# Optimization experiments

Hardware: AMD Instinct MI355X
Metric: run time of the kernel (lower is better)

The kernel has to match this reference:

```python
import jax, jax.numpy as jnp
import numpy as np

N, E, B, IN, H = 20000, 50000, 1024, 32, 64

def setup_inputs() -> dict:
    key = jax.random.key(0)
    ks = jax.random.split(key, 32)
    d = {}
    d["x"] = jax.random.normal(ks[0], (N, IN), jnp.float32)
    d["edge_index"] = jax.random.randint(ks[1], (2, E), 0, N)
    d["edge_attr"] = jax.random.uniform(ks[2], (E, 6), dtype=jnp.float32)
    d["batch"] = jnp.sort(jax.random.randint(ks[3], (N,), 0, B))
    d["t"] = jax.random.uniform(ks[4], (B, 1), dtype=jnp.float32)
    d["p"] = jax.random.uniform(ks[5], (B, 1), dtype=jnp.float32)
    d["num_graphs"] = B
    def lin(k, fan_in, shape):
        return jax.random.normal(k, shape, jnp.float32) * (1.0 / np.sqrt(fan_in))
    # lin0: IN -> H
    d["W0"] = lin(ks[6], IN, (IN, H)); d["b0"] = jnp.zeros((H,), jnp.float32)
    # edge MLP: 6 -> 64 -> H*H
    d["We1"] = lin(ks[7], 6, (6, 64)); d["be1"] = jnp.zeros((64,), jnp.float32)
    d["We2"] = lin(ks[8], 64, (64, H * H)); d["be2"] = jnp.zeros((H * H,), jnp.float32)
    # NNConv root weight + bias
    d["Wroot"] = lin(ks[9], H, (H, H)); d["bconv"] = jnp.zeros((H,), jnp.float32)
    # GRU (input H, hidden H), torch layout [3H, *] gate order r,z,n
    d["gru_wih"] = lin(ks[10], H, (3 * H, H)); d["gru_whh"] = lin(ks[11], H, (3 * H, H))
    d["gru_bih"] = jnp.zeros((3 * H,), jnp.float32); d["gru_bhh"] = jnp.zeros((3 * H,), jnp.float32)
    # Set2Set LSTM (input 2H, hidden H), torch layout [4H, *] gate order i,f,g,o
    d["l_wih"] = lin(ks[12], 2 * H, (4 * H, 2 * H)); d["l_whh"] = lin(ks[13], H, (4 * H, H))
    d["l_bih"] = jnp.zeros((4 * H,), jnp.float32); d["l_bhh"] = jnp.zeros((4 * H,), jnp.float32)
    # readout MLP
    d["W1"] = lin(ks[14], 2 * H + 2, (2 * H + 2, H)); d["b1"] = jnp.zeros((H,), jnp.float32)
    d["W2"] = lin(ks[15], H, (H, 64)); d["b2"] = jnp.zeros((64,), jnp.float32)
    d["W3"] = lin(ks[16], 64, (64, 1)); d["b3"] = jnp.zeros((1,), jnp.float32)
    return d


def reference(x, edge_attr, t, p, W0, b0, We1, be1, We2, be2, Wroot, bconv,
              gru_wih, gru_whh, gru_bih, gru_bhh, l_wih, l_whh, l_bih, l_bhh,
              W1, b1, W2, b2, W3, b3, edge_index, batch, num_graphs):
    n_nodes = x.shape[0]
    hdim = W0.shape[1]
    src, dst = edge_index[0], edge_index[1]

    out = jax.nn.relu(x @ W0 + b0)            # [N,H]
    h = out

    # edge MLP -> per-edge weight matrices [E,H,H] (edge_attr is loop-invariant)
    ew = (jax.nn.relu(edge_attr @ We1 + be1) @ We2 + be2).reshape(-1, hdim, hdim)

    for _ in range(4):
        # NNConv: gather source features, per-edge matmul, scatter-add to targets
        msg = jnp.einsum('eh,eho->eo', out[src], ew)                 # [E,H]
        agg = jax.ops.segment_sum(msg, dst, num_segments=n_nodes)    # [N,H]
        m = jax.nn.relu(agg + out @ Wroot + bconv)
        # GRU step (single timestep)
        gi = m @ gru_wih.T + gru_bih
        gh = h @ gru_whh.T + gru_bhh
        ir, iz, inn = jnp.split(gi, 3, axis=-1)
        hr, hz, hn = jnp.split(gh, 3, axis=-1)
        r = jax.nn.sigmoid(ir + hr)
        z = jax.nn.sigmoid(iz + hz)
        nn_ = jnp.tanh(inn + r * hn)
        h = (1.0 - z) * nn_ + z * h
        out = h

    # Set2Set pooling, 3 processing steps
    qh = jnp.zeros((num_graphs, hdim), x.dtype)
    qc = jnp.zeros((num_graphs, hdim), x.dtype)
    q_star = jnp.zeros((num_graphs, 2 * hdim), x.dtype)
    for _ in range(3):
        g = q_star @ l_wih.T + l_bih + qh @ l_whh.T + l_bhh
        gi_, gf_, gg_, go_ = jnp.split(g, 4, axis=-1)
        qc = jax.nn.sigmoid(gf_) * qc + jax.nn.sigmoid(gi_) * jnp.tanh(gg_)
        qh = jax.nn.sigmoid(go_) * jnp.tanh(qc)
        q = qh                                                        # [B,H]
        e = jnp.sum(out * q[batch], axis=-1, keepdims=True)          # [N,1]
        emax = jax.ops.segment_max(e, batch, num_segments=num_graphs)
        a = jnp.exp(e - emax[batch])
        asum = jax.ops.segment_sum(a, batch, num_segments=num_graphs)
        a = a / asum[batch]                                           # segment softmax
        r_ = jax.ops.segment_sum(a * out, batch, num_segments=num_graphs)
        q_star = jnp.concatenate([q, r_], axis=-1)

    feat = jnp.concatenate([q_star, t, p], axis=-1)                   # [B,2H+2]
    y = jax.nn.relu(feat @ W1 + b1)
    y = jax.nn.relu(y @ W2 + b2)
    y = y @ W3 + b3
    return y.reshape(-1)
```

## Files before the change

kernel.cpp:

```cpp
#include <hip/hip_runtime.h>
#include <math.h>

#define N_NODES 20000
#define N_EDGES 50000
#define NB      1024
#define IND     32
#define HDIM    64

typedef __attribute__((ext_vector_type(8))) short bf16x8;
typedef __attribute__((ext_vector_type(4))) float f32x4;

static inline size_t align_up(size_t x, size_t a) { return (x + a - 1) & ~(a - 1); }

__device__ __forceinline__ float sigmoidf_(float x) {
    return 1.0f / (1.0f + __expf(-x));
}
__device__ __forceinline__ float tanhf_(float x) {
    float xc = fminf(fmaxf(x, -15.0f), 15.0f);
    float e = __expf(2.0f * xc);
    return (e - 1.0f) / (e + 1.0f);
}
__device__ __forceinline__ unsigned pk2(float p0, float p1) {
    unsigned u0 = __float_as_uint(p0) + 0x8000u;
    unsigned u1 = __float_as_uint(p1) + 0x8000u;
    return __builtin_amdgcn_perm(u1, u0, 0x07060302u);
}
__device__ __forceinline__ unsigned bf1(float v) {
    return (__float_as_uint(v) + 0x8000u) >> 16;
}

__global__ void k_prep(const float* __restrict__ We2, const float* __restrict__ be2,
                       short* __restrict__ We2b,
                       const float* __restrict__ Wroot, const float* __restrict__ gwhh,
                       const float* __restrict__ gwih,
                       short* __restrict__ WB1h, short* __restrict__ WB1l,
                       short* __restrict__ WB2h, short* __restrict__ WB2l,
                       const float* __restrict__ lwih, const float* __restrict__ lwhh,
                       float* __restrict__ lwihT, float* __restrict__ lwhhT,
                       const int* __restrict__ batch, int* __restrict__ offs) {
    int bid = blockIdx.x, tid = threadIdx.x;
    if (bid < 1040) {
        int idx = bid * 256 + tid;
        int s = idx >> 12;
        int col = idx & 4095;
        int k = col >> 6, o = col & 63;
        float val = (s < 64) ? We2[k * 4096 + s * 64 + o] : be2[k * 64 + o];
        int dst = s * 4096 + (((o >> 4) * 128 + (k >> 5) * 64 + ((k >> 3) & 3) * 16 + (o & 15)) << 3) + (k & 7);
        We2b[dst] = (short)bf1(val);
    } else if (bid < 1152) {
        int idx = (bid - 1040) * 256 + tid;
        if (idx < 28672) {
            bool b1 = idx < 16384;
            int li = b1 ? idx : idx - 16384;
            int j = li & 7, lane = (li >> 3) & 63, c = (li >> 9) & 1, otile = li >> 10;
            int k = c * 32 + (lane >> 4) * 8 + j;
            int o = otile * 16 + (lane & 15);
            float val;
            if (b1) val = (o < 64) ? Wroot[k * 64 + o] : gwhh[(o - 64) * 64 + k];
            else    val = gwih[o * 64 + k];
            unsigned hs = bf1(val);
            float lo = val - __uint_as_float(hs << 16);
            unsigned ls = bf1(lo);
            if (b1) { WB1h[li] = (short)hs; WB1l[li] = (short)ls; }
            else    { WB2h[li] = (short)hs; WB2l[li] = (short)ls; }
        }
    } else if (bid < 1280) {
        int idx = (bid - 1152) * 256 + tid;
        int i = idx >> 8, j = idx & 255;
        lwihT[idx] = lwih[j * 128 + i];
    } else if (bid < 1344) {
        int idx = (bid - 1280) * 256 + tid;
        int i = idx >> 8, j = idx & 255;
        lwhhT[idx] = lwhh[j * 64 + i];
    } else {
        int i = (bid - 1344) * 256 + tid;
        if (i <= NB) {
            int lo = 0, hi = N_NODES;
            while (lo < hi) { int mid = (lo + hi) >> 1; if (batch[mid] < i) lo = mid + 1; else hi = mid; }
            offs[i] = lo;
        }
    }
}

__global__ void k_count(const int* __restrict__ ei, int* __restrict__ deg) {
    int e = blockIdx.x * 256 + threadIdx.x;
    if (e < N_EDGES) atomicAdd(&deg[ei[N_EDGES + e]], 1);
}

__global__ void k_scan(const int* __restrict__ deg, int* __restrict__ rowptr, int* __restrict__ cursor) {
    __shared__ int s_w[16];
    int t = threadIdx.x;
    int base = t * 20;
    int v[20]; int s = 0;
#pragma unroll
    for (int i = 0; i < 20; ++i) {
        int idx = base + i;
        v[i] = (idx < N_NODES) ? deg[idx] : 0;
        s += v[i];
    }
    int lane = t & 63, w = t >> 6;
    int inc = s;
#pragma unroll
    for (int off = 1; off < 64; off <<= 1) {
        int o = __shfl_up(inc, off);
        if (lane >= off) inc += o;
    }
    if (lane == 63) s_w[w] = inc;
    __syncthreads();
    if (w == 0 && lane < 16) {
        int x = s_w[lane];
        int xs = x;
#pragma unroll
        for (int off = 1; off < 16; off <<= 1) {
            int o = __shfl_up(xs, off);
            if (lane >= off) xs += o;
        }
        s_w[lane] = xs - x;
    }
    __syncthreads();
    int run = s_w[w] + (inc - s);
#pragma unroll
    for (int i = 0; i < 20; ++i) {
        int idx = base + i;
        if (idx < N_NODES) { rowptr[idx] = run; cursor[idx] = run; }
        else if (idx == N_NODES) rowptr[idx] = run;
        run += v[i];
    }
}

__global__ void k_fill(const int* __restrict__ ei, int* __restrict__ cursor, int* __restrict__ perm) {
    int e = blockIdx.x * 256 + threadIdx.x;
    if (e < N_EDGES) {
        int pos = atomicAdd(&cursor[ei[N_EDGES + e]], 1);
        perm[pos] = e;
    }
}

__global__ void k_init_feat(const float* __restrict__ x, const float* __restrict__ W0,
                            const float* __restrict__ b0, float* __restrict__ hbuf,
                            const float* __restrict__ ea, const float* __restrict__ We1,
                            const float* __restrict__ be1, float* __restrict__ re) {
    int bid = blockIdx.x;
    int tid = threadIdx.x;
    int w = tid >> 6, j = tid & 63;
    if (bid < 5000) {
        int n = bid * 4 + w;
        float acc = b0[j];
        const float* xr = x + n * IND;
#pragma unroll
        for (int i = 0; i < IND; ++i) acc = fmaf(xr[i], W0[i * 64 + j], acc);
        hbuf[n * 64 + j] = fmaxf(acc, 0.0f);
    } else {
        int e = (bid - 5000) * 4 + w;
        if (e >= N_EDGES) return;
        float acc = be1[j];
        const float* er = ea + e * 6;
#pragma unroll
        for (int i = 0; i < 6; ++i) acc = fmaf(er[i], We1[i * 64 + j], acc);
        re[e * 64 + j] = fmaxf(acc, 0.0f);
    }
}

__launch_bounds__(256, 3)
__global__ void k_msg_mfma(const float* __restrict__ hbuf, const float* __restrict__ reb,
                           const short* __restrict__ We2b, const int* __restrict__ ei,
                           float* __restrict__ msg) {
    __shared__ float s_v[64][64];
    int tid = threadIdx.x;
    int eb = blockIdx.x * 64;
    int lane = tid & 63;
    int w = tid >> 6;
    int l15 = lane & 15, lhi = lane >> 4;

    {
        int se = tid >> 2;
        int sh = tid & 3;
        int ge = eb + se;
        const float* rowp = (ge < N_EDGES) ? (hbuf + (size_t)ei[ge] * 64) : (const float*)0;
#pragma unroll
        for (int rr4 = 0; rr4 < 4; ++rr4) {
            int hb = rr4 * 16 + sh * 4;
            float4 vv = rowp ? *(const float4*)(rowp + hb) : make_float4(0.f, 0.f, 0.f, 0.f);
            s_v[hb + 0][se] = vv.x; s_v[hb + 1][se] = vv.y;
            s_v[hb + 2][se] = vv.z; s_v[hb + 3][se] = vv.w;
        }
    }

    union U { int4 i4; bf16x8 v; };
    U a_re[4][2];
#pragma unroll
    for (int m = 0; m < 4; ++m) {
        int ge = eb + m * 16 + l15;
        if (ge < N_EDGES) {
            const float* rp = reb + (size_t)ge * 64 + lhi * 8;
            float4 x0 = *(const float4*)(rp);
            float4 x1 = *(const float4*)(rp + 4);
            float4 y0 = *(const float4*)(rp + 32);
            float4 y1 = *(const float4*)(rp + 36);
            a_re[m][0].i4 = make_int4(pk2(x0.x, x0.y), pk2(x0.z, x0.w), pk2(x1.x, x1.y), pk2(x1.z, x1.w));
            a_re[m][1].i4 = make_int4(pk2(y0.x, y0.y), pk2(y0.z, y0.w), pk2(y1.x, y1.y), pk2(y1.z, y1.w));
        } else {
            a_re[m][0].i4 = make_int4(0, 0, 0, 0);
            a_re[m][1].i4 = make_int4(0, 0, 0, 0);
        }
    }

    const int4* bp0 = (const int4*)We2b + (w * 128 + lane);
    const int4* bp1 = bp0 + 64;
    int4 Sc0[4], Sc1[4];
#pragma unroll
    for (int j = 0; j < 4; ++j) {
        Sc0[j] = bp0[j * 512];
        Sc1[j] = bp1[j * 512];
    }

    __syncthreads();

    const f32x4 zero4 = {0.f, 0.f, 0.f, 0.f};
    f32x4 macc[4];
#pragma unroll
    for (int m = 0; m < 4; ++m) macc[m] = zero4;

    float4 vv[4], vn[4];
#pragma unroll
    for (int m = 0; m < 4; ++m) vv[m] = *(const float4*)&s_v[0][m * 16 + lhi * 4];

    for (int g = 0; g < 16; ++g) {
#pragma unroll
        for (int j = 0; j < 4; ++j) {
            int s = g * 4 + j;
            int snext = (s < 63) ? (s + 1) : 63;
#pragma unroll
            for (int m = 0; m < 4; ++m)
                vn[m] = *(const float4*)&s_v[snext][m * 16 + lhi * 4];
            U bb0, bb1; bb0.i4 = Sc0[j]; bb1.i4 = Sc1[j];
#pragma unroll
            for (int m = 0; m < 4; ++m) {
                f32x4 t = __builtin_amdgcn_mfma_f32_16x16x32_bf16(a_re[m][0].v, bb0.v, zero4, 0, 0, 0);
                t = __builtin_amdgcn_mfma_f32_16x16x32_bf16(a_re[m][1].v, bb1.v, t, 0, 0, 0);
                macc[m][0] = fmaf(vv[m].x, t[0], macc[m][0]);
                macc[m][1] = fmaf(vv[m].y, t[1], macc[m][1]);
                macc[m][2] = fmaf(vv[m].z, t[2], macc[m][2]);
                macc[m][3] = fmaf(vv[m].w, t[3], macc[m][3]);
            }
            int sload = (s + 4 <= 64) ? (s + 4) : 64;
            Sc0[j] = bp0[sload * 512];
            Sc1[j] = bp1[sload * 512];
#pragma unroll
            for (int m = 0; m < 4; ++m) vv[m] = vn[m];
        }
    }

    {
        U bb0, bb1; bb0.i4 = Sc0[0]; bb1.i4 = Sc1[0];
#pragma unroll
        for (int m = 0; m < 4; ++m) {
            int e = m * 16 + l15;
            U a0, a1;
            a0.i4 = make_int4(
                pk2(s_v[lhi * 8 + 0][e], s_v[lhi * 8 + 1][e]),
                pk2(s_v[lhi * 8 + 2][e], s_v[lhi * 8 + 3][e]),
                pk2(s_v[lhi * 8 + 4][e], s_v[lhi * 8 + 5][e]),
                pk2(s_v[lhi * 8 + 6][e], s_v[lhi * 8 + 7][e]));
            a1.i4 = make_int4(
                pk2(s_v[32 + lhi * 8 + 0][e], s_v[32 + lhi * 8 + 1][e]),
                pk2(s_v[32 + lhi * 8 + 2][e], s_v[32 + lhi * 8 + 3][e]),
                pk2(s_v[32 + lhi * 8 + 4][e], s_v[32 + lhi * 8 + 5][e]),
                pk2(s_v[32 + lhi * 8 + 6][e], s_v[32 + lhi * 8 + 7][e]));
            macc[m] = __builtin_amdgcn_mfma_f32_16x16x32_bf16(a0.v, bb0.v, macc[m], 0, 0, 0);
            macc[m] = __builtin_amdgcn_mfma_f32_16x16x32_bf16(a1.v, bb1.v, macc[m], 0, 0, 0);
        }
    }
    int o = w * 16 + l15;
#pragma unroll
    for (int m = 0; m < 4; ++m) {
#pragma unroll
        for (int r = 0; r < 4; ++r) {
            int el = m * 16 + lhi * 4 + r;
            int ge = eb + el;
            if (ge < N_EDGES) msg[(size_t)ge * 64 + o] = macc[m][r];
        }
    }
}

__launch_bounds__(256, 4)
__global__ void k_node_update(float* __restrict__ hbuf, const float* __restrict__ msg,
                              const int* __restrict__ rowptr, const int* __restrict__ perm,
                              const short* __restrict__ WB1h, const short* __restrict__ WB1l,
                              const short* __restrict__ WB2h, const short* __restrict__ WB2l,
                              const float* __restrict__ bconv, const float* __restrict__ bih,
                              const float* __restrict__ bhh) {
    __shared__ short s_hh[32][72];
    __shared__ short s_hl[32][72];
    __shared__ short s_mh[32][72];
    __shared__ short s_ml[32][72];
    __shared__ float s_agg[32][68];
    int tid = threadIdx.x;
    int nbase = blockIdx.x * 32;
    int lane = tid & 63, w = tid >> 6;
    int l15 = lane & 15, lhi = lane >> 4;

    {
        int nt = tid >> 3, q = tid & 7;
        int n = nbase + nt;
#pragma unroll
        for (int c4 = 0; c4 < 2; ++c4) {
            int col = q * 8 + c4 * 4;
            float4 v = *(const float4*)&hbuf[(size_t)n * 64 + col];
            unsigned h01 = pk2(v.x, v.y), h23 = pk2(v.z, v.w);
            float f0 = __uint_as_float(h01 << 16);
            float f1 = __uint_as_float(h01 & 0xffff0000u);
            float f2 = __uint_as_float(h23 << 16);
            float f3 = __uint_as_float(h23 & 0xffff0000u);
            unsigned l01 = pk2(v.x - f0, v.y - f1), l23 = pk2(v.z - f2, v.w - f3);
            *(unsigned*)&s_hh[nt][col]     = h01;
            *(unsigned*)&s_hh[nt][col + 2] = h23;
            *(unsigned*)&s_hl[nt][col]     = l01;
            *(unsigned*)&s_hl[nt][col + 2] = l23;
        }
        float4 aggv[2];
#pragma unroll
        for (int c4 = 0; c4 < 2; ++c4)
            aggv[c4] = *(const float4*)&bconv[q * 8 + c4 * 4];
        int rs = rowptr[n], rend = rowptr[n + 1];
        for (int qq = rs; qq < rend; ++qq) {
            const float* mrow = msg + (size_t)perm[qq] * 64 + q * 8;
#pragma unroll
            for (int c4 = 0; c4 < 2; ++c4) {
                float4 mv = *(const float4*)&mrow[c4 * 4];
                aggv[c4].x += mv.x; aggv[c4].y += mv.y;
                aggv[c4].z += mv.z; aggv[c4].w += mv.w;
            }
        }
#pragma unroll
        for (int c4 = 0; c4 < 2; ++c4)
            *(float4*)&s_agg[nt][q * 8 + c4 * 4] = aggv[c4];
    }
    __syncthreads();

    union U { int4 i4; bf16x8 v; };
    U ah[2][2], al[2][2];
#pragma unroll
    for (int m = 0; m < 2; ++m)
#pragma unroll
        for (int c = 0; c < 2; ++c) {
            ah[m][c].i4 = *(const int4*)&s_hh[m * 16 + l15][c * 32 + lhi * 8];
            al[m][c].i4 = *(const int4*)&s_hl[m * 16 + l15][c * 32 + lhi * 8];
        }

    const int4* B1h = (const int4*)WB1h;
    const int4* B1l = (const int4*)WB1l;
    const int4* B2h = (const int4*)WB2h;
    const int4* B2l = (const int4*)WB2l;

    f32x4 C0[2], G[3][2], I[3][2];

    {
        int ot = w;
        U bh0, bh1, bl0, bl1;
        bh0.i4 = B1h[(ot * 2 + 0) * 64 + lane];
        bh1.i4 = B1h[(ot * 2 + 1) * 64 + lane];
        bl0.i4 = B1l[(ot * 2 + 0) * 64 + lane];
        bl1.i4 = B1l[(ot * 2 + 1) * 64 + lane];
#pragma unroll
        for (int m = 0; m < 2; ++m) {
            f32x4 c;
#pragma unroll
            for (int r = 0; r < 4; ++r) c[r] = s_agg[m * 16 + lhi * 4 + r][w * 16 + l15];
            c = __builtin_amdgcn_mfma_f32_16x16x32_bf16(ah[m][0].v, bh0.v, c, 0, 0, 0);
            c = __builtin_amdgcn_mfma_f32_16x16x32_bf16(ah[m][1].v, bh1.v, c, 0, 0, 0);
            c = __builtin_amdgcn_mfma_f32_16x16x32_bf16(al[m][0].v, bh0.v, c, 0, 0, 0);
            c = __builtin_amdgcn_mfma_f32_16x16x32_bf16(al[m][1].v, bh1.v, c, 0, 0, 0);
            c = __builtin_amdgcn_mfma_f32_16x16x32_bf16(ah[m][0].v, bl0.v, c, 0, 0, 0);
            c = __builtin_amdgcn_mfma_f32_16x16x32_bf16(ah[m][1].v, bl1.v, c, 0, 0, 0);
            C0[m] = c;
        }
    }
#pragma unroll
    for (int m = 0; m < 2; ++m)
#pragma unroll
        for (int r = 0; r < 4; ++r) {
            float mv = fmaxf(C0[m][r], 0.0f);
            int row = m * 16 + lhi * 4 + r, col = w * 16 + l15;
            unsigned hs = bf1(mv);
            float lof = mv - __uint_as_float(hs << 16);
            s_mh[row][col] = (short)hs;
            s_ml[row][col] = (short)bf1(lof);
        }
#pragma unroll
    for (int p = 1; p < 4; ++p) {
        int ot = p * 4 + w;
        U bh0, bh1, bl0, bl1;
        bh0.i4 = B1h[(ot * 2 + 0) * 64 + lane];
        bh1.i4 = B1h[(ot * 2 + 1) * 64 + lane];
        bl0.i4 = B1l[(ot * 2 + 0) * 64 + lane];
        bl1.i4 = B1l[(ot * 2 + 1) * 64 + lane];
        float bv = bhh[(p - 1) * 64 + w * 16 + l15];
#pragma unroll
        for (int m = 0; m < 2; ++m) {
            f32x4 c = {bv, bv, bv, bv};
            c = __builtin_amdgcn_mfma_f32_16x16x32_bf16(ah[m][0].v, bh0.v, c, 0, 0, 0);
            c = __builtin_amdgcn_mfma_f32_16x16x32_bf16(ah[m][1].v, bh1.v, c, 0, 0, 0);
            c = __builtin_amdgcn_mfma_f32_16x16x32_bf16(al[m][0].v, bh0.v, c, 0, 0, 0);
            c = __builtin_amdgcn_mfma_f32_16x16x32_bf16(al[m][1].v, bh1.v, c, 0, 0, 0);
            c = __builtin_amdgcn_mfma_f32_16x16x32_bf16(ah[m][0].v, bl0.v, c, 0, 0, 0);
            c = __builtin_amdgcn_mfma_f32_16x16x32_bf16(ah[m][1].v, bl1.v, c, 0, 0, 0);
            G[p - 1][m] = c;
        }
    }
    __syncthreads();
    U mh[2][2], ml[2][2];
#pragma unroll
    for (int m = 0; m < 2; ++m)
#pragma unroll
        for (int c = 0; c < 2; ++c) {
            mh[m][c].i4 = *(const int4*)&s_mh[m * 16 + l15][c * 32 + lhi * 8];
            ml[m][c].i4 = *(const int4*)&s_ml[m * 16 + l15][c * 32 + lhi * 8];
        }
#pragma unroll
    for (int p = 0; p < 3; ++p) {
        int ot = p * 4 + w;
        U bh0, bh1, bl0, bl1;
        bh0.i4 = B2h[(ot * 2 + 0) * 64 + lane];
        bh1.i4 = B2h[(ot * 2 + 1) * 64 + lane];
        bl0.i4 = B2l[(ot * 2 + 0) * 64 + lane];
        bl1.i4 = B2l[(ot * 2 + 1) * 64 + lane];
        float bv = bih[p * 64 + w * 16 + l15];
#pragma unroll
        for (int m = 0; m < 2; ++m) {
            f32x4 c = {bv, bv, bv, bv};
            c = __builtin_amdgcn_mfma_f32_16x16x32_bf16(mh[m][0].v, bh0.v, c, 0, 0, 0);
            c = __builtin_amdgcn_mfma_f32_16x16x32_bf16(mh[m][1].v, bh1.v, c, 0, 0, 0);
            c = __builtin_amdgcn_mfma_f32_16x16x32_bf16(ml[m][0].v, bh0.v, c, 0, 0, 0);
            c = __builtin_amdgcn_mfma_f32_16x16x32_bf16(ml[m][1].v, bh1.v, c, 0, 0, 0);
            c = __builtin_amdgcn_mfma_f32_16x16x32_bf16(mh[m][0].v, bl0.v, c, 0, 0, 0);
            c = __builtin_amdgcn_mfma_f32_16x16x32_bf16(mh[m][1].v, bl1.v, c, 0, 0, 0);
            I[p][m] = c;
        }
    }
#pragma unroll
    for (int m = 0; m < 2; ++m)
#pragma unroll
        for (int r = 0; r < 4; ++r) {
            int row = m * 16 + lhi * 4 + r;
            int n = nbase + row;
            int col = w * 16 + l15;
            float hold = __uint_as_float(((unsigned)(unsigned short)s_hh[row][col]) << 16)
                       + __uint_as_float(((unsigned)(unsigned short)s_hl[row][col]) << 16);
            float rg = sigmoidf_(I[0][m][r] + G[0][m][r]);
            float z  = sigmoidf_(I[1][m][r] + G[1][m][r]);
            float nn = tanhf_(I[2][m][r] + rg * G[2][m][r]);
            hbuf[(size_t)n * 64 + col] = (1.0f - z) * nn + z * hold;
        }
}

__launch_bounds__(256)
__global__ void k_set2set(const float* __restrict__ hbuf, const int* __restrict__ offs,
                          const float* __restrict__ t, const float* __restrict__ p,
                          const float* __restrict__ lwihT, const float* __restrict__ lwhhT,
                          const float* __restrict__ l_bih, const float* __restrict__ l_bhh,
                          const float* __restrict__ W1, const float* __restrict__ b1,
                          const float* __restrict__ W2, const float* __restrict__ b2,
                          const float* __restrict__ W3, const float* __restrict__ b3,
                          float* __restrict__ y) {
    __shared__ float s_qs[192];
    __shared__ float s_g[256];
    __shared__ float s_racc[4][64];
    __shared__ float s_m[4], s_l[4];
    __shared__ float s_y[64];
    int b = blockIdx.x;
    int tid = threadIdx.x;
    int w = tid >> 6, lane = tid & 63;
    int s = offs[b], e = offs[b + 1];
    float bi = l_bih[tid] + l_bhh[tid];
    float qc = 0.f;

    if (tid < 192) s_qs[tid] = 0.f;
    __syncthreads();

    for (int iter = 0; iter < 3; ++iter) {
        float g = bi;
#pragma unroll 8
        for (int i = 0; i < 128; ++i) g = fmaf(s_qs[i], lwihT[i * 256 + tid], g);
#pragma unroll 8
        for (int i = 0; i < 64; ++i)  g = fmaf(s_qs[128 + i], lwhhT[i * 256 + tid], g);
        s_g[tid] = g;
        __syncthreads();
        if (w == 0) {
            float ci = sigmoidf_(s_g[lane]);
            float cf = sigmoidf_(s_g[64 + lane]);
            float cg = tanhf_(s_g[128 + lane]);
            float co = sigmoidf_(s_g[192 + lane]);
            qc = cf * qc + ci * cg;
            float qh = co * tanhf_(qc);
            s_qs[lane] = qh;
            s_qs[128 + lane] = qh;
        }
        __syncthreads();
        float qv = s_qs[128 + lane];
        float mx = -1e30f, l = 0.0f, racc = 0.0f;
        for (int n = s + w; n < e; n += 4) {
            float xv = hbuf[(size_t)n * 64 + lane];
            float prod = xv * qv;
#pragma unroll
            for (int off = 32; off > 0; off >>= 1) prod += __shfl_xor(prod, off);
            float mnew = fmaxf(mx, prod);
            float scale = __expf(mx - mnew);
            float wgt = __expf(prod - mnew);
            l = l * scale + wgt;
            racc = racc * scale + wgt * xv;
            mx = mnew;
        }
        s_racc[w][lane] = racc;
        if (lane == 0) { s_m[w] = mx; s_l[w] = l; }
        __syncthreads();
        if (w == 0) {
            float M = fmaxf(fmaxf(s_m[0], s_m[1]), fmaxf(s_m[2], s_m[3]));
            float L = 0.f, R = 0.f;
#pragma unroll
            for (int ww = 0; ww < 4; ++ww) {
                float sc = __expf(s_m[ww] - M);
                L += s_l[ww] * sc;
                R = fmaf(s_racc[ww][lane], sc, R);
            }
            s_qs[64 + lane] = (e > s) ? (R / L) : 0.0f;
        }
        __syncthreads();
    }
    if (w == 0) {
        float acc = b1[lane];
#pragma unroll 8
        for (int i = 0; i < 128; ++i) acc = fmaf(s_qs[i], W1[i * 64 + lane], acc);
        acc = fmaf(t[b], W1[128 * 64 + lane], acc);
        acc = fmaf(p[b], W1[129 * 64 + lane], acc);
        acc = fmaxf(acc, 0.0f);
        s_y[lane] = acc;
        float acc2 = b2[lane];
#pragma unroll 8
        for (int i = 0; i < 64; ++i) acc2 = fmaf(s_y[i], W2[i * 64 + lane], acc2);
        acc2 = fmaxf(acc2, 0.0f);
        float part = acc2 * W3[lane];
#pragma unroll
        for (int off = 32; off > 0; off >>= 1) part += __shfl_xor(part, off);
        if (lane == 0) y[b] = part + b3[0];
    }
}

extern "C" void kernel_launch(void* const* d_in, const int* in_sizes, int n_in,
                              void* d_out, int out_size, void* d_ws, size_t ws_size,
                              hipStream_t stream) {
    const float* x     = (const float*)d_in[0];
    const int*   ei    = (const int*)  d_in[1];
    const float* ea    = (const float*)d_in[2];
    const int*   batch = (const int*)  d_in[3];
    const float* t     = (const float*)d_in[4];
    const float* p     = (const float*)d_in[5];
    const float* W0    = (const float*)d_in[7];
    const float* b0    = (const float*)d_in[8];
    const float* We1   = (const float*)d_in[9];
    const float* be1   = (const float*)d_in[10];
    const float* We2   = (const float*)d_in[11];
    const float* be2   = (const float*)d_in[12];
    const float* Wroot = (const float*)d_in[13];
    const float* bconv = (const float*)d_in[14];
    const float* gwih  = (const float*)d_in[15];
    const float* gwhh  = (const float*)d_in[16];
    const float* gbih  = (const float*)d_in[17];
    const float* gbhh  = (const float*)d_in[18];
    const float* lwih  = (const float*)d_in[19];
    const float* lwhh  = (const float*)d_in[20];
    const float* lbih  = (const float*)d_in[21];
    const float* lbhh  = (const float*)d_in[22];
    const float* W1    = (const float*)d_in[23];
    const float* b1    = (const float*)d_in[24];
    const float* W2    = (const float*)d_in[25];
    const float* b2    = (const float*)d_in[26];
    const float* W3    = (const float*)d_in[27];
    const float* b3    = (const float*)d_in[28];
    float* y = (float*)d_out;

    char* ws = (char*)d_ws;
    size_t off = 0;
    auto alloc = [&](size_t nbytes) {
        void* ptr = (void*)(ws + off);
        off += align_up(nbytes, 256);
        return ptr;
    };
    float* hbuf   = (float*)alloc((size_t)N_NODES * 64 * 4);
    float* reb    = (float*)alloc((size_t)N_EDGES * 64 * 4);
    float* msg    = (float*)alloc((size_t)N_EDGES * 64 * 4);
    short* We2b   = (short*)alloc((size_t)65 * 4096 * 2);
    short* WB1h   = (short*)alloc(16384 * 2);
    short* WB1l   = (short*)alloc(16384 * 2);
    short* WB2h   = (short*)alloc(12288 * 2);
    short* WB2l   = (short*)alloc(12288 * 2);
    float* lwihT  = (float*)alloc(32768 * 4);
    float* lwhhT  = (float*)alloc(16384 * 4);
    int*   offs   = (int*)  alloc((NB + 1) * 4);
    int*   deg    = (int*)  alloc(N_NODES * 4);
    int*   rowptr = (int*)  alloc((N_NODES + 1) * 4);
    int*   cursor = (int*)  alloc(N_NODES * 4);
    int*   perm   = (int*)  alloc(N_EDGES * 4);

    k_prep<<<1349, 256, 0, stream>>>(We2, be2, We2b, Wroot, gwhh, gwih,
                                     WB1h, WB1l, WB2h, WB2l,
                                     lwih, lwhh, lwihT, lwhhT, batch, offs);
    hipMemsetAsync(deg, 0, (size_t)N_NODES * 4, stream);
    k_count<<<(N_EDGES + 255) / 256, 256, 0, stream>>>(ei, deg);
    k_scan<<<1, 1024, 0, stream>>>(deg, rowptr, cursor);
    k_fill<<<(N_EDGES + 255) / 256, 256, 0, stream>>>(ei, cursor, perm);

    k_init_feat<<<17500, 256, 0, stream>>>(x, W0, b0, hbuf, ea, We1, be1, reb);

    for (int it = 0; it < 4; ++it) {
        k_msg_mfma<<<(N_EDGES + 63) / 64, 256, 0, stream>>>(hbuf, reb, We2b, ei, msg);
        k_node_update<<<N_NODES / 32, 256, 0, stream>>>(hbuf, msg, rowptr, perm,
                                                        WB1h, WB1l, WB2h, WB2l,
                                                        bconv, gbih, gbhh);
    }

    k_set2set<<<NB, 256, 0, stream>>>(hbuf, offs, t, p, lwihT, lwhhT, lbih, lbhh,
                                      W1, b1, W2, b2, W3, b3, y);
}
```

Baseline: 414.1 us.

## Split message kernel reduction over hidden dim across two blocks with partial buffers

The per-edge message kernel now launches two blocks per 64-edge tile. Each block handles half of the 64 input hidden slices, and only one half adds the bias slab. The two partial messages are written to separate buffers, and the node update kernel sums both during aggregation. This doubles the parallelism of the MFMA-heavy message kernel, at the cost of duplicated gather and edge-feature loads per tile, an extra message buffer write, and double the message reads in node update.

```diff
diff --git a/kernel.cpp b/kernel.cpp
--- a/kernel.cpp
+++ b/kernel.cpp
@@ -164,10 +164,12 @@
 __launch_bounds__(256, 3)
 __global__ void k_msg_mfma(const float* __restrict__ hbuf, const float* __restrict__ reb,
                            const short* __restrict__ We2b, const int* __restrict__ ei,
-                           float* __restrict__ msg) {
+                           float* __restrict__ msgA, float* __restrict__ msgB) {
     __shared__ float s_v[64][64];
     int tid = threadIdx.x;
-    int eb = blockIdx.x * 64;
+    int tile = blockIdx.x >> 1;
+    int half = blockIdx.x & 1;
+    int eb = tile * 64;
     int lane = tid & 63;
     int w = tid >> 6;
     int l15 = lane & 15, lhi = lane >> 4;
@@ -205,13 +207,14 @@
         }
     }
 
+    int hbase = half * 32;
     const int4* bp0 = (const int4*)We2b + (w * 128 + lane);
     const int4* bp1 = bp0 + 64;
     int4 Sc0[4], Sc1[4];
 #pragma unroll
     for (int j = 0; j < 4; ++j) {
-        Sc0[j] = bp0[j * 512];
-        Sc1[j] = bp1[j * 512];
+        Sc0[j] = bp0[(size_t)(hbase + j) * 512];
+        Sc1[j] = bp1[(size_t)(hbase + j) * 512];
     }
 
     __syncthreads();
@@ -223,13 +226,13 @@
 
     float4 vv[4], vn[4];
 #pragma unroll
-    for (int m = 0; m < 4; ++m) vv[m] = *(const float4*)&s_v[0][m * 16 + lhi * 4];
-
-    for (int g = 0; g < 16; ++g) {
+    for (int m = 0; m < 4; ++m) vv[m] = *(const float4*)&s_v[hbase][m * 16 + lhi * 4];
+
+    for (int g = 0; g < 8; ++g) {
 #pragma unroll
         for (int j = 0; j < 4; ++j) {
             int s = g * 4 + j;
-            int snext = (s < 63) ? (s + 1) : 63;
+            int snext = (s < 31) ? (hbase + s + 1) : (hbase + 31);
 #pragma unroll
             for (int m = 0; m < 4; ++m)
                 vn[m] = *(const float4*)&s_v[snext][m * 16 + lhi * 4];
@@ -243,15 +246,16 @@
                 macc[m][2] = fmaf(vv[m].z, t[2], macc[m][2]);
                 macc[m][3] = fmaf(vv[m].w, t[3], macc[m][3]);
             }
-            int sload = (s + 4 <= 64) ? (s + 4) : 64;
-            Sc0[j] = bp0[sload * 512];
-            Sc1[j] = bp1[sload * 512];
+            int gslab = hbase + s + 4;
+            if (gslab > 64) gslab = 64;
+            Sc0[j] = bp0[(size_t)gslab * 512];
+            Sc1[j] = bp1[(size_t)gslab * 512];
 #pragma unroll
             for (int m = 0; m < 4; ++m) vv[m] = vn[m];
         }
     }
 
-    {
+    if (half == 1) {
         U bb0, bb1; bb0.i4 = Sc0[0]; bb1.i4 = Sc1[0];
 #pragma unroll
         for (int m = 0; m < 4; ++m) {
@@ -271,6 +275,7 @@
             macc[m] = __builtin_amdgcn_mfma_f32_16x16x32_bf16(a1.v, bb1.v, macc[m], 0, 0, 0);
         }
     }
+    float* mout = half ? msgB : msgA;
     int o = w * 16 + l15;
 #pragma unroll
     for (int m = 0; m < 4; ++m) {
@@ -278,13 +283,14 @@
         for (int r = 0; r < 4; ++r) {
             int el = m * 16 + lhi * 4 + r;
             int ge = eb + el;
-            if (ge < N_EDGES) msg[(size_t)ge * 64 + o] = macc[m][r];
+            if (ge < N_EDGES) mout[(size_t)ge * 64 + o] = macc[m][r];
         }
     }
 }
 
 __launch_bounds__(256, 4)
-__global__ void k_node_update(float* __restrict__ hbuf, const float* __restrict__ msg,
+__global__ void k_node_update(float* __restrict__ hbuf, const float* __restrict__ msgA,
+                              const float* __restrict__ msgB,
                               const int* __restrict__ rowptr, const int* __restrict__ perm,
                               const short* __restrict__ WB1h, const short* __restrict__ WB1l,
                               const short* __restrict__ WB2h, const short* __restrict__ WB2l,
@@ -324,12 +330,15 @@
             aggv[c4] = *(const float4*)&bconv[q * 8 + c4 * 4];
         int rs = rowptr[n], rend = rowptr[n + 1];
         for (int qq = rs; qq < rend; ++qq) {
-            const float* mrow = msg + (size_t)perm[qq] * 64 + q * 8;
+            size_t mbase = (size_t)perm[qq] * 64 + q * 8;
+            const float* mrowA = msgA + mbase;
+            const float* mrowB = msgB + mbase;
 #pragma unroll
             for (int c4 = 0; c4 < 2; ++c4) {
-                float4 mv = *(const float4*)&mrow[c4 * 4];
-                aggv[c4].x += mv.x; aggv[c4].y += mv.y;
-                aggv[c4].z += mv.z; aggv[c4].w += mv.w;
+                float4 ma = *(const float4*)&mrowA[c4 * 4];
+                float4 mb = *(const float4*)&mrowB[c4 * 4];
+                aggv[c4].x += ma.x + mb.x; aggv[c4].y += ma.y + mb.y;
+                aggv[c4].z += ma.z + mb.z; aggv[c4].w += ma.w + mb.w;
             }
         }
 #pragma unroll
@@ -588,7 +597,8 @@
     };
     float* hbuf   = (float*)alloc((size_t)N_NODES * 64 * 4);
     float* reb    = (float*)alloc((size_t)N_EDGES * 64 * 4);
-    float* msg    = (float*)alloc((size_t)N_EDGES * 64 * 4);
+    float* msgA   = (float*)alloc((size_t)N_EDGES * 64 * 4);
+    float* msgB   = (float*)alloc((size_t)N_EDGES * 64 * 4);
     short* We2b   = (short*)alloc((size_t)65 * 4096 * 2);
     short* WB1h   = (short*)alloc(16384 * 2);
     short* WB1l   = (short*)alloc(16384 * 2);
@@ -612,9 +622,10 @@
 
     k_init_feat<<<17500, 256, 0, stream>>>(x, W0, b0, hbuf, ea, We1, be1, reb);
 
+    int tiles = (N_EDGES + 63) / 64;
     for (int it = 0; it < 4; ++it) {
-        k_msg_mfma<<<(N_EDGES + 63) / 64, 256, 0, stream>>>(hbuf, reb, We2b, ei, msg);
-        k_node_update<<<N_NODES / 32, 256, 0, stream>>>(hbuf, msg, rowptr, perm,
+        k_msg_mfma<<<tiles * 2, 256, 0, stream>>>(hbuf, reb, We2b, ei, msgA, msgB);
+        k_node_update<<<N_NODES / 32, 256, 0, stream>>>(hbuf, msgA, msgB, rowptr, perm,
                                                         WB1h, WB1l, WB2h, WB2l,
                                                         bconv, gbih, gbhh);
     }
```

Result: slower. 469.4 us (+13.3%).
